# Kernel tuning notes

Hardware: AMD Instinct MI355X
Metric: run time of the kernel (lower is better)

Reference implementation:

```python
import jax, jax.numpy as jnp
import numpy as np

NUM_HEADS = 16
NUM_GROUPS = 2
HEAD_DIM = 128  # in_features // num_heads = 2048 // 16
MAX_POS = 512 + 256 + 256  # MAX_SEQ_LEN + SHARED_SLOTS + OUTPUT_SLOTS


def _rope_tables():
    inv_freq = 1.0 / 10000 ** (jnp.arange(0, HEAD_DIM, 2) / HEAD_DIM)
    t = jnp.arange(MAX_POS)
    freqs = jnp.outer(t, inv_freq)
    freqs = jnp.concatenate([freqs, freqs], axis=-1)  # [MAX_POS, HEAD_DIM]
    return jnp.sin(freqs), jnp.cos(freqs)


def _rotate_half(x):
    h = x.shape[-1] // 2
    x1, x2 = x[..., :h], x[..., h:]
    return jnp.concatenate([-x2, x1], axis=-1)


def setup_inputs() -> dict:
    key = jax.random.key(0)
    ks = jax.random.split(key, 5)
    b, s, d = 4, 1024, 2048
    kvd = NUM_GROUPS * HEAD_DIM
    sc = 1.0 / np.sqrt(d).astype(np.float32)
    return {
        "x": jax.random.normal(ks[0], (b, s, d), jnp.float32),
        "Wq": jax.random.normal(ks[1], (d, d), jnp.float32) * sc,
        "bq": jnp.zeros((d,), jnp.float32),
        "Wk": jax.random.normal(ks[2], (d, kvd), jnp.float32) * sc,
        "bk": jnp.zeros((kvd,), jnp.float32),
        "Wv": jax.random.normal(ks[3], (d, kvd), jnp.float32) * sc,
        "bv": jnp.zeros((kvd,), jnp.float32),
        "Wo": jax.random.normal(ks[4], (d, d), jnp.float32) * sc,
        "bo": jnp.zeros((d,), jnp.float32),
    }


def reference(x, Wq, bq, Wk, bk, Wv, bv, Wo, bo):
    b, s, d = x.shape
    sin, cos = _rope_tables()
    # original: sin_cached[q_pos, None, :] broadcasts over (b, s, heads, head_dim)
    sin = sin[:s][None, :, None, :]
    cos = cos[:s][None, :, None, :]

    q = (x @ Wq + bq).reshape(b, s, NUM_HEADS, HEAD_DIM)
    k = (x @ Wk + bk).reshape(b, s, NUM_GROUPS, HEAD_DIM)
    v = (x @ Wv + bv).reshape(b, s, NUM_GROUPS, HEAD_DIM)

    q = q * cos + _rotate_half(q) * sin
    k = k * cos + _rotate_half(k) * sin

    # GQA: avoid materializing expanded K/V by grouping the head dim of q.
    r = NUM_HEADS // NUM_GROUPS  # repeats per group
    qg = q.reshape(b, s, NUM_GROUPS, r, HEAD_DIM)
    scale = HEAD_DIM ** -0.5
    scores = jnp.einsum('bsgrd,btgd->bgrst', qg, k) * scale
    attn = jax.nn.softmax(scores, axis=-1)
    out = jnp.einsum('bgrst,btgd->bsgrd', attn, v).reshape(b, s, d)
    return out @ Wo + bo
```

## Files before the change

### kernel.cpp

```cpp
#include <hip/hip_runtime.h>
#include <hip/hip_bf16.h>
#include <hip/hip_fp16.h>
#include <math.h>

#define BATCH   4
#define SEQ     1024
#define DMODEL  2048
#define NHEADS  16
#define NGROUPS 2
#define HDIM    128
#define ROWS    (BATCH * SEQ)
#define NQKV    2560

typedef float    f32x4 __attribute__((ext_vector_type(4)));
typedef _Float16 f16x8 __attribute__((ext_vector_type(8)));

__device__ __forceinline__ void glds16(const void* g, void* s) {
    __builtin_amdgcn_global_load_lds(
        (__attribute__((address_space(1))) void*)g,
        (__attribute__((address_space(3))) void*)s, 16, 0, 0);
}

__global__ void rope_table_kernel(float* __restrict__ sin_t, float* __restrict__ cos_t) {
    int idx = blockIdx.x * 256 + threadIdx.x;
    int p = idx >> 6, j = idx & 63;
    float inv = powf(10000.0f, -(float)j * (1.0f / 64.0f));
    float f = (float)p * inv;
    sin_t[idx] = sinf(f);
    cos_t[idx] = cosf(f);
}

__global__ void convert_x_kernel(const float* __restrict__ x, _Float16* __restrict__ xo) {
    int i = (blockIdx.x * 256 + threadIdx.x) * 8;
    float v[8];
    *reinterpret_cast<float4*>(&v[0]) = *reinterpret_cast<const float4*>(x + i);
    *reinterpret_cast<float4*>(&v[4]) = *reinterpret_cast<const float4*>(x + i + 4);
    f16x8 h;
#pragma unroll
    for (int j = 0; j < 8; ++j) h[j] = (_Float16)v[j];
    *reinterpret_cast<f16x8*>(xo + i) = h;
}

__global__ __launch_bounds__(256)
void transpose_w_kernel(const float* __restrict__ W, int ldw,
                        _Float16* __restrict__ dst, int drow0, int K) {
    __shared__ float tile[64][65];
    int n0 = blockIdx.x * 64, k0 = blockIdx.y * 64;
#pragma unroll
    for (int it = 0; it < 16; ++it) {
        int e = it * 256 + threadIdx.x;
        int r = e >> 6, c = e & 63;
        tile[r][c] = W[(size_t)(k0 + r) * ldw + n0 + c];
    }
    __syncthreads();
#pragma unroll
    for (int it = 0; it < 16; ++it) {
        int e = it * 256 + threadIdx.x;
        int nr = e >> 6, kc = e & 63;
        dst[(size_t)(drow0 + n0 + nr) * K + k0 + kc] = (_Float16)tile[kc][nr];
    }
}

__global__ void bias_cat_kernel(const float* __restrict__ bq, const float* __restrict__ bk,
                                const float* __restrict__ bv, float* __restrict__ bc) {
    int i = blockIdx.x * 256 + threadIdx.x;
    if (i >= NQKV) return;
    bc[i] = (i < 2048) ? bq[i] : ((i < 2304) ? bk[i - 2048] : bv[i - 2304]);
}

template<int OUT_HALF>
__global__ __launch_bounds__(256, 3)
void gemm_fp16_kernel(const _Float16* __restrict__ A, const _Float16* __restrict__ Bt,
                      const float* __restrict__ bias, void* __restrict__ Cout,
                      int M, int N, int K) {
    __shared__ __align__(16) _Float16 lds[16384];
    _Float16* As = lds;
    _Float16* Bs = lds + 8192;

    const int tid  = threadIdx.x;
    const int lane = tid & 63;
    const int w    = tid >> 6;
    const int nbn  = N >> 7;
    const int nwg  = gridDim.x;
    const int cpx  = nwg >> 3;
    const int bid  = blockIdx.x;
    const int swz  = (bid & 7) * cpx + (bid >> 3);
    const int row0 = (swz / nbn) << 7;
    const int col0 = (swz % nbn) << 7;
    const int wr   = (w >> 1) << 6;
    const int wc   = (w & 1) << 6;

    const f32x4 fz = {0.f, 0.f, 0.f, 0.f};
    f32x4 acc[4][4];
#pragma unroll
    for (int i = 0; i < 4; ++i)
#pragma unroll
        for (int j = 0; j < 4; ++j) acc[i][j] = fz;

    for (int k0 = 0; k0 < K; k0 += 64) {
        __syncthreads();
#pragma unroll
        for (int it = 0; it < 4; ++it) {
            int chunk = it * 256 + tid;
            int trow  = chunk >> 3;
            int jp    = chunk & 7;
            int j     = jp ^ (trow & 7);
            size_t aoff = (size_t)(row0 + trow) * K + k0 + j * 8;
            size_t boff = (size_t)(col0 + trow) * K + k0 + j * 8;
            int ldst = (it * 256 + (tid & 192)) * 16;
            glds16(A  + aoff, (char*)As + ldst);
            glds16(Bt + boff, (char*)Bs + ldst);
        }
        __syncthreads();

#pragma unroll
        for (int ks = 0; ks < 2; ++ks) {
            f16x8 a4[4], b4[4];
            int ja = ks * 4 + (lane >> 4);
#pragma unroll
            for (int i = 0; i < 4; ++i) {
                int ar = wr + i * 16 + (lane & 15);
                a4[i] = *reinterpret_cast<const f16x8*>(
                    (const char*)As + ar * 128 + ((ja ^ (ar & 7)) << 4));
                int br = wc + i * 16 + (lane & 15);
                b4[i] = *reinterpret_cast<const f16x8*>(
                    (const char*)Bs + br * 128 + ((ja ^ (br & 7)) << 4));
            }
#pragma unroll
            for (int i = 0; i < 4; ++i)
#pragma unroll
                for (int j = 0; j < 4; ++j)
                    acc[i][j] = __builtin_amdgcn_mfma_f32_16x16x32_f16(a4[i], b4[j], acc[i][j], 0, 0, 0);
        }
    }

    float bv4[4];
#pragma unroll
    for (int j = 0; j < 4; ++j) bv4[j] = bias[col0 + wc + j * 16 + (lane & 15)];
#pragma unroll
    for (int i = 0; i < 4; ++i)
#pragma unroll
        for (int j = 0; j < 4; ++j)
#pragma unroll
            for (int r = 0; r < 4; ++r) {
                int grow = row0 + wr + i * 16 + ((lane >> 4) << 2) + r;
                int gcol = col0 + wc + j * 16 + (lane & 15);
                float v = acc[i][j][r] + bv4[j];
                if (OUT_HALF)
                    ((_Float16*)Cout)[(size_t)grow * N + gcol] = (_Float16)v;
                else
                    ((float*)Cout)[(size_t)grow * N + gcol] = v;
            }
}

__global__ void rope_qk_kernel(const _Float16* __restrict__ qkv,
                               const float* __restrict__ sin_t, const float* __restrict__ cos_t,
                               _Float16* __restrict__ qh, _Float16* __restrict__ kh) {
    int idx = blockIdx.x * 256 + threadIdx.x;
    int jc = idx & 7, t = idx >> 3;
    int j0 = jc * 8;
    const int NQ = ROWS * NHEADS;
    const _Float16* src;
    _Float16* dst;
    int s;
    float qsc;
    if (t < NQ) {
        int row = t >> 4, h = t & 15;
        int b = row >> 10; s = row & 1023;
        src = qkv + (size_t)row * NQKV + h * HDIM;
        dst = qh + ((size_t)(b * NHEADS + h) * SEQ + s) * HDIM;
        qsc = 0.08838834764831845f;
    } else {
        int t2 = t - NQ;
        int row = t2 >> 1, g = t2 & 1;
        int b = row >> 10; s = row & 1023;
        src = qkv + (size_t)row * NQKV + 2048 + g * HDIM;
        dst = kh + ((size_t)(b * NGROUPS + g) * SEQ + s) * HDIM;
        qsc = 1.0f;
    }
    f16x8 x1 = *reinterpret_cast<const f16x8*>(src + j0);
    f16x8 x2 = *reinterpret_cast<const f16x8*>(src + j0 + 64);
    float cc[8], ss[8];
    *reinterpret_cast<float4*>(&cc[0]) = *reinterpret_cast<const float4*>(cos_t + s * 64 + j0);
    *reinterpret_cast<float4*>(&cc[4]) = *reinterpret_cast<const float4*>(cos_t + s * 64 + j0 + 4);
    *reinterpret_cast<float4*>(&ss[0]) = *reinterpret_cast<const float4*>(sin_t + s * 64 + j0);
    *reinterpret_cast<float4*>(&ss[4]) = *reinterpret_cast<const float4*>(sin_t + s * 64 + j0 + 4);
    f16x8 o1, o2;
#pragma unroll
    for (int j = 0; j < 8; ++j) {
        float f1 = (float)x1[j], f2 = (float)x2[j];
        o1[j] = (_Float16)((f1 * cc[j] - f2 * ss[j]) * qsc);
        o2[j] = (_Float16)((f2 * cc[j] + f1 * ss[j]) * qsc);
    }
    *reinterpret_cast<f16x8*>(dst + j0)      = o1;
    *reinterpret_cast<f16x8*>(dst + j0 + 64) = o2;
}

__global__ __launch_bounds__(256)
void transpose_v_kernel(const _Float16* __restrict__ qkv, _Float16* __restrict__ vt) {
    __shared__ _Float16 tile[64][72];
    int s0 = blockIdx.x * 64, d0 = blockIdx.y * 64, bg = blockIdx.z;
    int b = bg >> 1, g = bg & 1;
#pragma unroll
    for (int it = 0; it < 2; ++it) {
        int c = it * 256 + threadIdx.x;
        int r = c >> 3, cc = (c & 7) * 8;
        f16x8 v = *reinterpret_cast<const f16x8*>(
            qkv + (size_t)(b * SEQ + s0 + r) * NQKV + 2304 + g * HDIM + d0 + cc);
#pragma unroll
        for (int j = 0; j < 8; ++j) tile[r][cc + j] = v[j];
    }
    __syncthreads();
#pragma unroll
    for (int it = 0; it < 2; ++it) {
        int c = it * 256 + threadIdx.x;
        int dr = c >> 3, sc = (c & 7) * 8;
        f16x8 o;
#pragma unroll
        for (int j = 0; j < 8; ++j) o[j] = tile[sc + j][dr];
        *reinterpret_cast<f16x8*>(vt + ((size_t)bg * HDIM + d0 + dr) * SEQ + s0 + sc) = o;
    }
}

__global__ __launch_bounds__(256, 2)
void attn_kernel(const _Float16* __restrict__ qh, const _Float16* __restrict__ kh,
                 const _Float16* __restrict__ vt, _Float16* __restrict__ ao) {
    __shared__ __align__(16) char smem[57344];
    char* Qs = smem;
    char* Ks = smem + 16384;
    char* Vs = smem + 32768;
    char* Ps = smem + 49152;

    const int tid = threadIdx.x, lane = tid & 63, w = tid >> 6;
    const int qt0 = blockIdx.x << 6;
    const int h = blockIdx.y, b = blockIdx.z;
    const int g = h >> 3;
    const _Float16* qbase = qh + ((size_t)(b * NHEADS + h) * SEQ + qt0) * HDIM;
    const _Float16* kbase = kh + (size_t)(b * NGROUPS + g) * SEQ * HDIM;
    const _Float16* vbase = vt + (size_t)(b * NGROUPS + g) * HDIM * SEQ;

#pragma unroll
    for (int it = 0; it < 4; ++it) {
        int c = it * 256 + tid;
        int row = c >> 4, jc = c & 15;
        int sj = jc ^ (row & 7);
        glds16((const char*)(qbase + (size_t)row * HDIM) + (sj << 4),
               Qs + (it * 256 + (tid & 192)) * 16);
    }

    float m_run[4] = {-1e30f, -1e30f, -1e30f, -1e30f};
    float l_run[4] = {0.f, 0.f, 0.f, 0.f};
    const f32x4 fz = {0.f, 0.f, 0.f, 0.f};
    f32x4 oacc[8];
#pragma unroll
    for (int i = 0; i < 8; ++i) oacc[i] = fz;

    const int qrow  = w * 16 + (lane & 15);
    const int qroff = qrow * 256;
    const int qswz  = qrow & 7;
    char* Pw = Ps + w * 2048;
    const int prow  = lane & 15;
    const int pswz  = prow & 7;

    for (int t0 = 0; t0 < SEQ; t0 += 64) {
        __syncthreads();
#pragma unroll
        for (int it = 0; it < 4; ++it) {
            int c = it * 256 + tid;
            int row = c >> 4, jc = c & 15;
            int sj = jc ^ (row & 7);
            glds16((const char*)(kbase + (size_t)(t0 + row) * HDIM) + (sj << 4),
                   Ks + (it * 256 + (tid & 192)) * 16);
        }
#pragma unroll
        for (int it = 0; it < 4; ++it) {
            int c = it * 256 + tid;
            int d = c >> 3, jc = c & 7;
            int sj = jc ^ (d & 7);
            glds16((const char*)(vbase + (size_t)d * SEQ + t0) + (sj << 4),
                   Vs + (it * 256 + (tid & 192)) * 16);
        }
        __syncthreads();

        f32x4 sacc[4];
#pragma unroll
        for (int i = 0; i < 4; ++i) sacc[i] = fz;
#pragma unroll
        for (int ks = 0; ks < 4; ++ks) {
            int chA = ks * 4 + (lane >> 4);
            f16x8 af = *reinterpret_cast<const f16x8*>(Qs + qroff + ((chA ^ qswz) << 4));
#pragma unroll
            for (int nf = 0; nf < 4; ++nf) {
                int trow = nf * 16 + (lane & 15);
                f16x8 bf = *reinterpret_cast<const f16x8*>(
                    Ks + trow * 256 + (((ks * 4 + (lane >> 4)) ^ (trow & 7)) << 4));
                sacc[nf] = __builtin_amdgcn_mfma_f32_16x16x32_f16(af, bf, sacc[nf], 0, 0, 0);
            }
        }

        float mnew[4], scl[4], psum[4];
#pragma unroll
        for (int r = 0; r < 4; ++r) {
            float pm = fmaxf(fmaxf(sacc[0][r], sacc[1][r]), fmaxf(sacc[2][r], sacc[3][r]));
            pm = fmaxf(pm, __shfl_xor(pm, 1, 16));
            pm = fmaxf(pm, __shfl_xor(pm, 2, 16));
            pm = fmaxf(pm, __shfl_xor(pm, 4, 16));
            pm = fmaxf(pm, __shfl_xor(pm, 8, 16));
            mnew[r] = fmaxf(m_run[r], pm);
            scl[r] = __expf(m_run[r] - mnew[r]);
            m_run[r] = mnew[r];
            psum[r] = 0.f;
        }
#pragma unroll
        for (int nf = 0; nf < 4; ++nf)
#pragma unroll
            for (int r = 0; r < 4; ++r) {
                float p = __expf(sacc[nf][r] - mnew[r]);
                sacc[nf][r] = p;
                psum[r] += p;
            }
#pragma unroll
        for (int r = 0; r < 4; ++r) {
            float ps = psum[r];
            ps += __shfl_xor(ps, 1, 16);
            ps += __shfl_xor(ps, 2, 16);
            ps += __shfl_xor(ps, 4, 16);
            ps += __shfl_xor(ps, 8, 16);
            l_run[r] = l_run[r] * scl[r] + ps;
        }
#pragma unroll
        for (int i = 0; i < 8; ++i) {
            f32x4 o = oacc[i];
            o[0] *= scl[0]; o[1] *= scl[1]; o[2] *= scl[2]; o[3] *= scl[3];
            oacc[i] = o;
        }

#pragma unroll
        for (int nf = 0; nf < 4; ++nf)
#pragma unroll
            for (int r = 0; r < 4; ++r) {
                int pr = ((lane >> 4) << 2) + r;
                int pc = nf * 16 + (lane & 15);
                int byte = pr * 128 + ((pc * 2) ^ ((pr & 7) << 4));
                *reinterpret_cast<_Float16*>(Pw + byte) = (_Float16)sacc[nf][r];
            }

#pragma unroll
        for (int ks = 0; ks < 2; ++ks) {
            int chP = ks * 4 + (lane >> 4);
            f16x8 pa = *reinterpret_cast<const f16x8*>(Pw + prow * 128 + ((chP ^ pswz) << 4));
#pragma unroll
            for (int nf = 0; nf < 8; ++nf) {
                int vrow = nf * 16 + (lane & 15);
                f16x8 vf = *reinterpret_cast<const f16x8*>(
                    Vs + vrow * 128 + (((ks * 4 + (lane >> 4)) ^ (vrow & 7)) << 4));
                oacc[nf] = __builtin_amdgcn_mfma_f32_16x16x32_f16(pa, vf, oacc[nf], 0, 0, 0);
            }
        }
    }

#pragma unroll
    for (int nf = 0; nf < 8; ++nf)
#pragma unroll
        for (int r = 0; r < 4; ++r) {
            int qr  = qt0 + w * 16 + ((lane >> 4) << 2) + r;
            int col = h * HDIM + nf * 16 + (lane & 15);
            float v = oacc[nf][r] / l_run[r];
            ao[(size_t)(b * SEQ + qr) * DMODEL + col] = (_Float16)v;
        }
}

extern "C" void kernel_launch(void* const* d_in, const int* in_sizes, int n_in,
                              void* d_out, int out_size, void* d_ws, size_t ws_size,
                              hipStream_t stream) {
    const float* x  = (const float*)d_in[0];
    const float* Wq = (const float*)d_in[1];
    const float* bq = (const float*)d_in[2];
    const float* Wk = (const float*)d_in[3];
    const float* bk = (const float*)d_in[4];
    const float* Wv = (const float*)d_in[5];
    const float* bv = (const float*)d_in[6];
    const float* Wo = (const float*)d_in[7];
    const float* bo = (const float*)d_in[8];
    float* out = (float*)d_out;

    char* ws = (char*)d_ws;
    _Float16* xs     = (_Float16*)(ws);
    _Float16* wqkv16 = (_Float16*)(ws + 16777216);
    _Float16* wot16  = (_Float16*)(ws + 27262976);
    _Float16* qkv16  = (_Float16*)(ws + 35651584);
    _Float16* qhb    = (_Float16*)(ws + 56623104);
    _Float16* khb    = (_Float16*)(ws + 73400320);
    _Float16* vtb    = (_Float16*)(ws + 75497472);
    float*    sint   = (float*)(ws + 77594624);
    float*    cost   = (float*)(ws + 77856768);
    float*    bias_c = (float*)(ws + 78118912);
    _Float16* ao = xs;

    rope_table_kernel<<<SEQ * 64 / 256, 256, 0, stream>>>(sint, cost);
    convert_x_kernel<<<ROWS * DMODEL / 8 / 256, 256, 0, stream>>>(x, xs);
    transpose_w_kernel<<<dim3(32, 32), 256, 0, stream>>>(Wq, DMODEL, wqkv16, 0, DMODEL);
    transpose_w_kernel<<<dim3(4, 32),  256, 0, stream>>>(Wk, 256,    wqkv16, 2048, DMODEL);
    transpose_w_kernel<<<dim3(4, 32),  256, 0, stream>>>(Wv, 256,    wqkv16, 2304, DMODEL);
    transpose_w_kernel<<<dim3(32, 32), 256, 0, stream>>>(Wo, DMODEL, wot16,  0, DMODEL);
    bias_cat_kernel<<<10, 256, 0, stream>>>(bq, bk, bv, bias_c);

    gemm_fp16_kernel<1><<<(ROWS / 128) * (NQKV / 128), 256, 0, stream>>>(
        xs, wqkv16, bias_c, qkv16, ROWS, NQKV, DMODEL);

    rope_qk_kernel<<<(ROWS * (NHEADS + NGROUPS) * 8) / 256, 256, 0, stream>>>(
        qkv16, sint, cost, qhb, khb);
    transpose_v_kernel<<<dim3(SEQ / 64, HDIM / 64, BATCH * NGROUPS), 256, 0, stream>>>(qkv16, vtb);

    attn_kernel<<<dim3(SEQ / 64, NHEADS, BATCH), 256, 0, stream>>>(qhb, khb, vtb, ao);

    gemm_fp16_kernel<0><<<(ROWS / 128) * (DMODEL / 128), 256, 0, stream>>>(
        ao, wot16, bo, out, ROWS, DMODEL, DMODEL);
}
```

Before: 324.9 us.

## Fuse Q RoPE into attention, double-buffer K/V, and lazily rescale softmax

The attention kernel now reads Q straight from the QKV projection output, applies RoPE and the softmax scale in registers, and keeps Q fragments in registers. This removes the separate Q rotation pass and its intermediate buffer. K/V tiles are double-buffered in shared memory, with the next tile's loads issued before computing on the current one. The online softmax skips rescaling of the accumulator unless the running max grows by more than a threshold. Shared memory use rises and register pressure increases from holding Q.

```diff
diff --git a/kernel.cpp b/kernel.cpp
--- a/kernel.cpp
+++ b/kernel.cpp
@@ -153,31 +153,16 @@
             }
 }
 
-__global__ void rope_qk_kernel(const _Float16* __restrict__ qkv,
-                               const float* __restrict__ sin_t, const float* __restrict__ cos_t,
-                               _Float16* __restrict__ qh, _Float16* __restrict__ kh) {
+__global__ void rope_k_kernel(const _Float16* __restrict__ qkv,
+                              const float* __restrict__ sin_t, const float* __restrict__ cos_t,
+                              _Float16* __restrict__ kh) {
     int idx = blockIdx.x * 256 + threadIdx.x;
     int jc = idx & 7, t = idx >> 3;
     int j0 = jc * 8;
-    const int NQ = ROWS * NHEADS;
-    const _Float16* src;
-    _Float16* dst;
-    int s;
-    float qsc;
-    if (t < NQ) {
-        int row = t >> 4, h = t & 15;
-        int b = row >> 10; s = row & 1023;
-        src = qkv + (size_t)row * NQKV + h * HDIM;
-        dst = qh + ((size_t)(b * NHEADS + h) * SEQ + s) * HDIM;
-        qsc = 0.08838834764831845f;
-    } else {
-        int t2 = t - NQ;
-        int row = t2 >> 1, g = t2 & 1;
-        int b = row >> 10; s = row & 1023;
-        src = qkv + (size_t)row * NQKV + 2048 + g * HDIM;
-        dst = kh + ((size_t)(b * NGROUPS + g) * SEQ + s) * HDIM;
-        qsc = 1.0f;
-    }
+    int row = t >> 1, g = t & 1;
+    int b = row >> 10, s = row & 1023;
+    const _Float16* src = qkv + (size_t)row * NQKV + 2048 + g * HDIM;
+    _Float16* dst = kh + ((size_t)(b * NGROUPS + g) * SEQ + s) * HDIM;
     f16x8 x1 = *reinterpret_cast<const f16x8*>(src + j0);
     f16x8 x2 = *reinterpret_cast<const f16x8*>(src + j0 + 64);
     float cc[8], ss[8];
@@ -189,8 +174,8 @@
 #pragma unroll
     for (int j = 0; j < 8; ++j) {
         float f1 = (float)x1[j], f2 = (float)x2[j];
-        o1[j] = (_Float16)((f1 * cc[j] - f2 * ss[j]) * qsc);
-        o2[j] = (_Float16)((f2 * cc[j] + f1 * ss[j]) * qsc);
+        o1[j] = (_Float16)(f1 * cc[j] - f2 * ss[j]);
+        o2[j] = (_Float16)(f2 * cc[j] + f1 * ss[j]);
     }
     *reinterpret_cast<f16x8*>(dst + j0)      = o1;
     *reinterpret_cast<f16x8*>(dst + j0 + 64) = o2;
@@ -223,29 +208,64 @@
 }
 
 __global__ __launch_bounds__(256, 2)
-void attn_kernel(const _Float16* __restrict__ qh, const _Float16* __restrict__ kh,
-                 const _Float16* __restrict__ vt, _Float16* __restrict__ ao) {
-    __shared__ __align__(16) char smem[57344];
-    char* Qs = smem;
-    char* Ks = smem + 16384;
-    char* Vs = smem + 32768;
-    char* Ps = smem + 49152;
+void attn_kernel(const _Float16* __restrict__ qkv, const _Float16* __restrict__ kh,
+                 const _Float16* __restrict__ vt,
+                 const float* __restrict__ sin_t, const float* __restrict__ cos_t,
+                 _Float16* __restrict__ ao) {
+    __shared__ __align__(16) char smem[73728];
 
     const int tid = threadIdx.x, lane = tid & 63, w = tid >> 6;
     const int qt0 = blockIdx.x << 6;
     const int h = blockIdx.y, b = blockIdx.z;
     const int g = h >> 3;
-    const _Float16* qbase = qh + ((size_t)(b * NHEADS + h) * SEQ + qt0) * HDIM;
     const _Float16* kbase = kh + (size_t)(b * NGROUPS + g) * SEQ * HDIM;
     const _Float16* vbase = vt + (size_t)(b * NGROUPS + g) * HDIM * SEQ;
 
-#pragma unroll
-    for (int it = 0; it < 4; ++it) {
-        int c = it * 256 + tid;
-        int row = c >> 4, jc = c & 15;
-        int sj = jc ^ (row & 7);
-        glds16((const char*)(qbase + (size_t)row * HDIM) + (sj << 4),
-               Qs + (it * 256 + (tid & 192)) * 16);
+    {
+        char* Kb = smem;
+        char* Vb = smem + 16384;
+#pragma unroll
+        for (int it = 0; it < 4; ++it) {
+            int c = it * 256 + tid;
+            int row = c >> 4, jc = c & 15;
+            int sj = jc ^ (row & 7);
+            glds16((const char*)(kbase + (size_t)row * HDIM) + (sj << 4),
+                   Kb + (it * 256 + (tid & 192)) * 16);
+        }
+#pragma unroll
+        for (int it = 0; it < 4; ++it) {
+            int c = it * 256 + tid;
+            int d = c >> 3, jc = c & 7;
+            int sj = jc ^ (d & 7);
+            glds16((const char*)(vbase + (size_t)d * SEQ) + (sj << 4),
+                   Vb + (it * 256 + (tid & 192)) * 16);
+        }
+    }
+
+    const int srow = qt0 + w * 16 + (lane & 15);
+    const int sl   = lane >> 4;
+    const _Float16* qrp = qkv + (size_t)(b * SEQ + srow) * NQKV + h * HDIM;
+    f16x8 af[4];
+#pragma unroll
+    for (int ks = 0; ks < 4; ++ks)
+        af[ks] = *reinterpret_cast<const f16x8*>(qrp + (ks * 4 + sl) * 8);
+    {
+        const float qsc = 0.08838834764831845f;
+#pragma unroll
+        for (int ks = 0; ks < 2; ++ks) {
+            int d0 = (ks * 4 + sl) * 8;
+            float cc[8], ss[8];
+            *reinterpret_cast<float4*>(&cc[0]) = *reinterpret_cast<const float4*>(cos_t + srow * 64 + d0);
+            *reinterpret_cast<float4*>(&cc[4]) = *reinterpret_cast<const float4*>(cos_t + srow * 64 + d0 + 4);
+            *reinterpret_cast<float4*>(&ss[0]) = *reinterpret_cast<const float4*>(sin_t + srow * 64 + d0);
+            *reinterpret_cast<float4*>(&ss[4]) = *reinterpret_cast<const float4*>(sin_t + srow * 64 + d0 + 4);
+#pragma unroll
+            for (int j = 0; j < 8; ++j) {
+                float f1 = (float)af[ks][j], f2 = (float)af[ks + 2][j];
+                af[ks][j]     = (_Float16)((f1 * cc[j] - f2 * ss[j]) * qsc);
+                af[ks + 2][j] = (_Float16)((f2 * cc[j] + f1 * ss[j]) * qsc);
+            }
+        }
     }
 
     float m_run[4] = {-1e30f, -1e30f, -1e30f, -1e30f};
@@ -255,67 +275,88 @@
 #pragma unroll
     for (int i = 0; i < 8; ++i) oacc[i] = fz;
 
-    const int qrow  = w * 16 + (lane & 15);
-    const int qroff = qrow * 256;
-    const int qswz  = qrow & 7;
-    char* Pw = Ps + w * 2048;
-    const int prow  = lane & 15;
-    const int pswz  = prow & 7;
-
-    for (int t0 = 0; t0 < SEQ; t0 += 64) {
-        __syncthreads();
-#pragma unroll
-        for (int it = 0; it < 4; ++it) {
-            int c = it * 256 + tid;
-            int row = c >> 4, jc = c & 15;
-            int sj = jc ^ (row & 7);
-            glds16((const char*)(kbase + (size_t)(t0 + row) * HDIM) + (sj << 4),
-                   Ks + (it * 256 + (tid & 192)) * 16);
-        }
-#pragma unroll
-        for (int it = 0; it < 4; ++it) {
-            int c = it * 256 + tid;
-            int d = c >> 3, jc = c & 7;
-            int sj = jc ^ (d & 7);
-            glds16((const char*)(vbase + (size_t)d * SEQ + t0) + (sj << 4),
-                   Vs + (it * 256 + (tid & 192)) * 16);
-        }
-        __syncthreads();
+    char* Pw = smem + 65536 + w * 2048;
+    const int prow = lane & 15;
+    const int pswz = prow & 7;
+
+    int cur = 0;
+    for (int t = 0; t < SEQ / 64; ++t) {
+        char* Kb = smem + (cur << 15);
+        char* Vb = Kb + 16384;
+        if (t < SEQ / 64 - 1) {
+            char* Kn = smem + ((cur ^ 1) << 15);
+            char* Vn = Kn + 16384;
+            int t0n = (t + 1) << 6;
+#pragma unroll
+            for (int it = 0; it < 4; ++it) {
+                int c = it * 256 + tid;
+                int row = c >> 4, jc = c & 15;
+                int sj = jc ^ (row & 7);
+                glds16((const char*)(kbase + (size_t)(t0n + row) * HDIM) + (sj << 4),
+                       Kn + (it * 256 + (tid & 192)) * 16);
+            }
+#pragma unroll
+            for (int it = 0; it < 4; ++it) {
+                int c = it * 256 + tid;
+                int d = c >> 3, jc = c & 7;
+                int sj = jc ^ (d & 7);
+                glds16((const char*)(vbase + (size_t)d * SEQ + t0n) + (sj << 4),
+                       Vn + (it * 256 + (tid & 192)) * 16);
+            }
+            asm volatile("s_waitcnt vmcnt(8)" ::: "memory");
+        } else {
+            asm volatile("s_waitcnt vmcnt(0)" ::: "memory");
+        }
+        asm volatile("s_barrier" ::: "memory");
 
         f32x4 sacc[4];
 #pragma unroll
         for (int i = 0; i < 4; ++i) sacc[i] = fz;
 #pragma unroll
         for (int ks = 0; ks < 4; ++ks) {
-            int chA = ks * 4 + (lane >> 4);
-            f16x8 af = *reinterpret_cast<const f16x8*>(Qs + qroff + ((chA ^ qswz) << 4));
 #pragma unroll
             for (int nf = 0; nf < 4; ++nf) {
                 int trow = nf * 16 + (lane & 15);
                 f16x8 bf = *reinterpret_cast<const f16x8*>(
-                    Ks + trow * 256 + (((ks * 4 + (lane >> 4)) ^ (trow & 7)) << 4));
-                sacc[nf] = __builtin_amdgcn_mfma_f32_16x16x32_f16(af, bf, sacc[nf], 0, 0, 0);
-            }
-        }
-
-        float mnew[4], scl[4], psum[4];
+                    Kb + trow * 256 + (((ks * 4 + (lane >> 4)) ^ (trow & 7)) << 4));
+                sacc[nf] = __builtin_amdgcn_mfma_f32_16x16x32_f16(af[ks], bf, sacc[nf], 0, 0, 0);
+            }
+        }
+
+        float pm[4];
 #pragma unroll
         for (int r = 0; r < 4; ++r) {
-            float pm = fmaxf(fmaxf(sacc[0][r], sacc[1][r]), fmaxf(sacc[2][r], sacc[3][r]));
-            pm = fmaxf(pm, __shfl_xor(pm, 1, 16));
-            pm = fmaxf(pm, __shfl_xor(pm, 2, 16));
-            pm = fmaxf(pm, __shfl_xor(pm, 4, 16));
-            pm = fmaxf(pm, __shfl_xor(pm, 8, 16));
-            mnew[r] = fmaxf(m_run[r], pm);
-            scl[r] = __expf(m_run[r] - mnew[r]);
-            m_run[r] = mnew[r];
-            psum[r] = 0.f;
-        }
+            float v = fmaxf(fmaxf(sacc[0][r], sacc[1][r]), fmaxf(sacc[2][r], sacc[3][r]));
+            v = fmaxf(v, __shfl_xor(v, 1, 16));
+            v = fmaxf(v, __shfl_xor(v, 2, 16));
+            v = fmaxf(v, __shfl_xor(v, 4, 16));
+            v = fmaxf(v, __shfl_xor(v, 8, 16));
+            pm[r] = v;
+        }
+        float growth = fmaxf(fmaxf(pm[0] - m_run[0], pm[1] - m_run[1]),
+                             fmaxf(pm[2] - m_run[2], pm[3] - m_run[3]));
+        if (__any(growth > 8.0f)) {
+            float scl[4];
+#pragma unroll
+            for (int r = 0; r < 4; ++r) {
+                float mn = fmaxf(m_run[r], pm[r]);
+                scl[r] = __expf(m_run[r] - mn);
+                m_run[r] = mn;
+                l_run[r] *= scl[r];
+            }
+#pragma unroll
+            for (int i = 0; i < 8; ++i) {
+                f32x4 o = oacc[i];
+                o[0] *= scl[0]; o[1] *= scl[1]; o[2] *= scl[2]; o[3] *= scl[3];
+                oacc[i] = o;
+            }
+        }
+        float psum[4] = {0.f, 0.f, 0.f, 0.f};
 #pragma unroll
         for (int nf = 0; nf < 4; ++nf)
 #pragma unroll
             for (int r = 0; r < 4; ++r) {
-                float p = __expf(sacc[nf][r] - mnew[r]);
+                float p = __expf(sacc[nf][r] - m_run[r]);
                 sacc[nf][r] = p;
                 psum[r] += p;
             }
@@ -326,13 +367,7 @@
             ps += __shfl_xor(ps, 2, 16);
             ps += __shfl_xor(ps, 4, 16);
             ps += __shfl_xor(ps, 8, 16);
-            l_run[r] = l_run[r] * scl[r] + ps;
-        }
-#pragma unroll
-        for (int i = 0; i < 8; ++i) {
-            f32x4 o = oacc[i];
-            o[0] *= scl[0]; o[1] *= scl[1]; o[2] *= scl[2]; o[3] *= scl[3];
-            oacc[i] = o;
+            l_run[r] += ps;
         }
 
 #pragma unroll
@@ -353,10 +388,13 @@
             for (int nf = 0; nf < 8; ++nf) {
                 int vrow = nf * 16 + (lane & 15);
                 f16x8 vf = *reinterpret_cast<const f16x8*>(
-                    Vs + vrow * 128 + (((ks * 4 + (lane >> 4)) ^ (vrow & 7)) << 4));
+                    Vb + vrow * 128 + (((ks * 4 + (lane >> 4)) ^ (vrow & 7)) << 4));
                 oacc[nf] = __builtin_amdgcn_mfma_f32_16x16x32_f16(pa, vf, oacc[nf], 0, 0, 0);
             }
         }
+
+        asm volatile("s_barrier" ::: "memory");
+        cur ^= 1;
     }
 
 #pragma unroll
@@ -389,12 +427,11 @@
     _Float16* wqkv16 = (_Float16*)(ws + 16777216);
     _Float16* wot16  = (_Float16*)(ws + 27262976);
     _Float16* qkv16  = (_Float16*)(ws + 35651584);
-    _Float16* qhb    = (_Float16*)(ws + 56623104);
-    _Float16* khb    = (_Float16*)(ws + 73400320);
-    _Float16* vtb    = (_Float16*)(ws + 75497472);
-    float*    sint   = (float*)(ws + 77594624);
-    float*    cost   = (float*)(ws + 77856768);
-    float*    bias_c = (float*)(ws + 78118912);
+    _Float16* khb    = (_Float16*)(ws + 56623104);
+    _Float16* vtb    = (_Float16*)(ws + 58720256);
+    float*    sint   = (float*)(ws + 60817408);
+    float*    cost   = (float*)(ws + 61079552);
+    float*    bias_c = (float*)(ws + 61341696);
     _Float16* ao = xs;
 
     rope_table_kernel<<<SEQ * 64 / 256, 256, 0, stream>>>(sint, cost);
@@ -408,11 +445,11 @@
     gemm_fp16_kernel<1><<<(ROWS / 128) * (NQKV / 128), 256, 0, stream>>>(
         xs, wqkv16, bias_c, qkv16, ROWS, NQKV, DMODEL);
 
-    rope_qk_kernel<<<(ROWS * (NHEADS + NGROUPS) * 8) / 256, 256, 0, stream>>>(
-        qkv16, sint, cost, qhb, khb);
+    rope_k_kernel<<<(ROWS * NGROUPS * 8) / 256, 256, 0, stream>>>(qkv16, sint, cost, khb);
     transpose_v_kernel<<<dim3(SEQ / 64, HDIM / 64, BATCH * NGROUPS), 256, 0, stream>>>(qkv16, vtb);
 
-    attn_kernel<<<dim3(SEQ / 64, NHEADS, BATCH), 256, 0, stream>>>(qhb, khb, vtb, ao);
+    attn_kernel<<<dim3(SEQ / 64, NHEADS, BATCH), 256, 0, stream>>>(
+        qkv16, khb, vtb, sint, cost, ao);
 
     gemm_fp16_kernel<0><<<(ROWS / 128) * (DMODEL / 128), 256, 0, stream>>>(
         ao, wot16, bo, out, ROWS, DMODEL, DMODEL);
```

New measurement: 318.9 us. No clear change (-1.9%).
